# Kernel optimization log

Hardware: AMD Instinct MI355X
Metric: run time of the kernel (lower is better)

The kernel has to match this reference:

```python
import jax, jax.numpy as jnp
import numpy as np

EMB, NW, H, L, FF, VOCAB, BS = 512, 64, 8, 4, 2048, 50257, 16


def setup_inputs() -> dict:
    key = jax.random.key(0)
    ks = jax.random.split(key, 8)
    d = EMB
    def n(k, shape, s=0.02):
        return jax.random.normal(k, shape, jnp.float32) * s
    return {
        "w_emb": jax.random.normal(ks[0], (BS, NW, d), jnp.float32),
        "table": jax.random.normal(ks[1], (VOCAB, d), jnp.float32) * 0.02,
        "word_enc": n(ks[2], (NW + 1, d)),            # learned token encodings
        "Wqkv": n(ks[3], (L, 3 * d, d)),              # in_proj per layer
        "bqkv": jnp.zeros((L, 3 * d), jnp.float32),
        "Wo": n(ks[4], (L, d, d)),
        "bo": jnp.zeros((L, d), jnp.float32),
        "W1": n(ks[5], (L, FF, d)),
        "b1": jnp.zeros((L, FF), jnp.float32),
        "W2": n(ks[6], (L, d, FF)),
        "b2": jnp.zeros((L, d), jnp.float32),
        "g1": jnp.ones((L, d), jnp.float32),
        "be1": jnp.zeros((L, d), jnp.float32),
        "g2": jnp.ones((L, d), jnp.float32),
        "be2": jnp.zeros((L, d), jnp.float32),
    }


def _ln(x, g, b, eps=1e-5):
    m = x.mean(-1, keepdims=True)
    v = ((x - m) ** 2).mean(-1, keepdims=True)
    return (x - m) * jax.lax.rsqrt(v + eps) * g + b


def reference(w_emb, table, word_enc, Wqkv, bqkv, Wo, bo, W1, b1, W2, b2, g1, be1, g2, be2):
    bs, _, d = w_emb.shape
    dh = d // H
    scale = 1.0 / np.sqrt(dh).astype(np.float32)
    # prepend zero token, add learned encodings -> (bs, NW+1, d)
    x = jnp.concatenate([jnp.zeros((bs, 1, d), w_emb.dtype), w_emb], axis=1) + word_enc
    for l in range(L):
        # self-attention (post-LN TransformerEncoderLayer, ReLU FFN)
        qkv = x @ Wqkv[l].T + bqkv[l]
        q, k, v = jnp.split(qkv, 3, axis=-1)
        s = x.shape[1]
        q = q.reshape(bs, s, H, dh)
        k = k.reshape(bs, s, H, dh)
        v = v.reshape(bs, s, H, dh)
        att = jax.nn.softmax(jnp.einsum('bqhd,bkhd->bhqk', q, k) * scale, axis=-1)
        ctx = jnp.einsum('bhqk,bkhd->bqhd', att, v).reshape(bs, s, d)
        x = _ln(x + ctx @ Wo[l].T + bo[l], g1[l], be1[l])
        h = jax.nn.relu(x @ W1[l].T + b1[l])
        x = _ln(x + h @ W2[l].T + b2[l], g2[l], be2[l])
    out = x[:, :-1]                                   # drop last position -> (bs, NW, d)
    # linear lookup: (out * table).sum(-1) == out @ table.T
    return jnp.einsum('bnd,vd->bnv', out, table)
```

## Files before the change

### kernel.cpp

```cpp
#include <hip/hip_runtime.h>
#include <hip/hip_bf16.h>

#define EMB 512
#define NW  64
#define SEQ 65
#define NH  8
#define DH  64
#define NL  4
#define FF_ 2048
#define VOCAB 50257
#define BS  16
#define TOK (BS*SEQ)
#define TOUT (BS*NW)

typedef short short8  __attribute__((ext_vector_type(8)));
typedef unsigned short ushort8n __attribute__((ext_vector_type(8)));
typedef float f32x4   __attribute__((ext_vector_type(4)));

__device__ __forceinline__ unsigned short f2bf(float f) {
    unsigned u = __float_as_uint(f);
    return (unsigned short)((u + 0x7FFF + ((u >> 16) & 1)) >> 16);
}

template<int N> __device__ __forceinline__ void wait_vm() {
    asm volatile("s_waitcnt vmcnt(%0)" :: "n"(N) : "memory");
}

constexpr int ilog2c(int v) { return v == 32 ? 5 : v == 64 ? 6 : v == 128 ? 7 : 0; }

#define SZ_WQKV (NL*3*EMB*EMB)
#define SZ_WO   (NL*EMB*EMB)
#define SZ_W1   (NL*FF_*EMB)
#define SZ_W2   (NL*EMB*FF_)
#define SZ_TAB  (VOCAB*EMB)
#define CVT_TOTAL (SZ_WQKV+SZ_WO+SZ_W1+SZ_W2+SZ_TAB)
#define O_WO   (SZ_WQKV)
#define O_W1   (O_WO+SZ_WO)
#define O_W2   (O_W1+SZ_W1)
#define O_TAB  (O_W2+SZ_W2)

__global__ void cvt_kernel(const float* __restrict__ wqkv, const float* __restrict__ wo,
                           const float* __restrict__ w1, const float* __restrict__ w2,
                           const float* __restrict__ table, unsigned short* __restrict__ dst) {
    const int U = CVT_TOTAL / 8;
    for (int u = blockIdx.x * blockDim.x + threadIdx.x; u < U; u += gridDim.x * blockDim.x) {
        size_t elem = (size_t)u * 8;
        const float* src; size_t loc = elem;
        if      (elem < O_WO)  { src = wqkv; }
        else if (elem < O_W1)  { src = wo;    loc = elem - O_WO; }
        else if (elem < O_W2)  { src = w1;    loc = elem - O_W1; }
        else if (elem < O_TAB) { src = w2;    loc = elem - O_W2; }
        else                   { src = table; loc = elem - O_TAB; }
        float4 f0 = *(const float4*)(src + loc);
        float4 f1 = *(const float4*)(src + loc + 4);
        ushort8n o;
        o[0]=f2bf(f0.x); o[1]=f2bf(f0.y); o[2]=f2bf(f0.z); o[3]=f2bf(f0.w);
        o[4]=f2bf(f1.x); o[5]=f2bf(f1.y); o[6]=f2bf(f1.z); o[7]=f2bf(f1.w);
        *(ushort8n*)(dst + elem) = o;
    }
}

__global__ void embed_kernel(const float* __restrict__ w_emb,
                             const float* __restrict__ word_enc,
                             float* __restrict__ x32,
                             unsigned short* __restrict__ x16) {
    int idx = blockIdx.x * blockDim.x + threadIdx.x;
    const int total = BS * SEQ * EMB;
    if (idx >= total) return;
    int d = idx & (EMB - 1);
    int s = (idx >> 9) % SEQ;
    int b = idx / (SEQ * EMB);
    float we = word_enc[s * EMB + d];
    float e = (s == 0) ? 0.f : w_emb[((size_t)b * NW + (s - 1)) * EMB + d];
    float v = e + we;
    x32[idx] = v;
    x16[idx] = f2bf(v);
}

template<int TM, int TN, int BK, int OUT_BF16, int RELU, int COMPACT, int SPLITK>
__global__ __launch_bounds__(256) void gemm4(const unsigned short* __restrict__ A,
                                             const unsigned short* __restrict__ B,
                                             const float* __restrict__ bias,
                                             void* __restrict__ C0,
                                             void* __restrict__ C1,
                                             const float* __restrict__ res,
                                             int M, int N, int K, int lda, int ldb) {
    constexpr int LTM = ilog2c(TM);
    constexpr int LTN = ilog2c(TN);
    constexpr int FR  = TM / 32, FC = TN / 32;
    constexpr int WRH = TM / 2,  WCH = TN / 2;
    constexpr int KCH = BK / 32;
    constexpr int AI  = (TM * BK) / (8 * 256);
    constexpr int BI  = (TN * BK) / (8 * 256);
    constexpr int L   = AI + BI;
    constexpr int ASZ = TM * BK * 2;
    constexpr int STRIDE = (TM + TN) * BK * 2;
    __shared__ __align__(16) char smem[3 * STRIDE];

    int t = threadIdx.x;
    int w = t >> 6, l = t & 63;
    int wr = w >> 1, wc = w & 1;
    int lr = l & 15, lh = l >> 4;

    int mtiles = (M + TM - 1) / TM;
    int ntiles = (N + TN - 1) / TN;
    int bid = blockIdx.x;
    int nchunk = gridDim.x >> 3;
    int lin = (bid & 7) * nchunk + (bid >> 3);
    int part = 0;
    if (SPLITK) { int tpp = mtiles * ntiles; part = (lin >= tpp); lin -= part * tpp; }
    int m0 = (lin % mtiles) * TM;
    int n0 = (lin / mtiles) * TN;

    const unsigned short* Ap = A + (size_t)part * K;
    const unsigned short* Bp = B + (size_t)part * K;
    float* Cf = (float*)(part ? C1 : C0);
    const float* biasp = (SPLITK && part) ? nullptr : bias;
    const float* resp  = (SPLITK && part) ? nullptr : res;

    f32x4 acc[FR][FC] = {};
    const int nt = K / BK;

    auto stageA = [&](int kt, int p) {
        char* dst = smem + p * STRIDE;
        #pragma unroll
        for (int i = 0; i < AI; ++i) {
            int tt = i * 256 + t;
            int row = tt & (TM - 1);
            int slot = tt >> LTM;
            int gr = m0 + row;
            if (COMPACT) gr = ((gr >> 6) * SEQ) + (gr & 63);
            else if (gr >= M) gr = M - 1;
            const unsigned short* gp = Ap + (size_t)gr * lda + kt + slot * 8;
            __builtin_amdgcn_global_load_lds(
                (const __attribute__((address_space(1))) void*)gp,
                (__attribute__((address_space(3))) void*)(dst + (size_t)(i * 256 + w * 64) * 16),
                16, 0, 0);
        }
    };
    auto stageB = [&](int kt, int p) {
        char* dst = smem + p * STRIDE + ASZ;
        #pragma unroll
        for (int i = 0; i < BI; ++i) {
            int tt = i * 256 + t;
            int row = tt & (TN - 1);
            int slot = tt >> LTN;
            int gr = n0 + row;
            if (gr >= N) gr = N - 1;
            const unsigned short* gp = Bp + (size_t)gr * ldb + kt + slot * 8;
            __builtin_amdgcn_global_load_lds(
                (const __attribute__((address_space(1))) void*)gp,
                (__attribute__((address_space(3))) void*)(dst + (size_t)(i * 256 + w * 64) * 16),
                16, 0, 0);
        }
    };
    auto compute = [&](int p) {
        const unsigned short* as_ = (const unsigned short*)(smem + p * STRIDE);
        const unsigned short* bs_ = as_ + TM * BK;
        #pragma unroll
        for (int kk = 0; kk < KCH; ++kk) {
            short8 af[FR], bfv[FC];
            #pragma unroll
            for (int mi = 0; mi < FR; ++mi)
                af[mi] = *(const short8*)(as_ + ((size_t)(kk * 4 + lh) * TM + wr * WRH + mi * 16 + lr) * 8);
            #pragma unroll
            for (int ni = 0; ni < FC; ++ni)
                bfv[ni] = *(const short8*)(bs_ + ((size_t)(kk * 4 + lh) * TN + wc * WCH + ni * 16 + lr) * 8);
            #pragma unroll
            for (int mi = 0; mi < FR; ++mi)
                #pragma unroll
                for (int ni = 0; ni < FC; ++ni)
                    acc[mi][ni] = __builtin_amdgcn_mfma_f32_16x16x32_bf16(af[mi], bfv[ni], acc[mi][ni], 0, 0, 0);
        }
    };

    stageA(0, 0); stageB(0, 0);
    if (nt > 1) { stageA(BK, 1); stageB(BK, 1); }

    for (int it = 0; it < nt; ++it) {
        if (it + 1 < nt) wait_vm<L>(); else wait_vm<0>();
        __builtin_amdgcn_s_barrier();
        __builtin_amdgcn_sched_barrier(0);
        if (it + 2 < nt) {
            stageA((it + 2) * BK, (it + 2) % 3);
            stageB((it + 2) * BK, (it + 2) % 3);
        }
        __builtin_amdgcn_s_setprio(1);
        compute(it % 3);
        __builtin_amdgcn_s_setprio(0);
        __builtin_amdgcn_sched_barrier(0);
    }

    if (OUT_BF16) {
        #pragma unroll
        for (int ni = 0; ni < FC; ++ni) {
            int gcol = n0 + wc * WCH + ni * 16 + lr;
            if (gcol >= N) continue;
            float bv = biasp ? biasp[gcol] : 0.f;
            #pragma unroll
            for (int mi = 0; mi < FR; ++mi)
                #pragma unroll
                for (int r = 0; r < 4; ++r) {
                    int grow = m0 + wr * WRH + mi * 16 + lh * 4 + r;
                    if (grow >= M) continue;
                    float v = acc[mi][ni][r] + bv;
                    if (RELU) v = fmaxf(v, 0.f);
                    ((unsigned short*)C0)[(size_t)grow * N + gcol] = f2bf(v);
                }
        }
    } else {
        __syncthreads();
        constexpr int PAD = WCH + 4;
        constexpr int CPR = WCH / 4;
        constexpr int J   = (16 * CPR) / 64;
        float* ep = (float*)smem + (size_t)w * 16 * PAD;
        #pragma unroll
        for (int mi = 0; mi < FR; ++mi) {
            asm volatile("s_waitcnt lgkmcnt(0)" ::: "memory");
            __builtin_amdgcn_sched_barrier(0);
            #pragma unroll
            for (int ni = 0; ni < FC; ++ni)
                #pragma unroll
                for (int r = 0; r < 4; ++r)
                    ep[(lh * 4 + r) * PAD + ni * 16 + lr] = acc[mi][ni][r];
            asm volatile("s_waitcnt lgkmcnt(0)" ::: "memory");
            __builtin_amdgcn_sched_barrier(0);
            #pragma unroll
            for (int j = 0; j < J; ++j) {
                int f4  = j * 64 + l;
                int row = f4 / CPR;
                int c4  = f4 % CPR;
                int grow = m0 + wr * WRH + mi * 16 + row;
                int gc   = n0 + wc * WCH + c4 * 4;
                if (grow < M) {
                    float4 v = *(const float4*)(ep + row * PAD + c4 * 4);
                    if (gc + 3 < N) {
                        if (biasp) {
                            float4 b4 = *(const float4*)(biasp + gc);
                            v.x += b4.x; v.y += b4.y; v.z += b4.z; v.w += b4.w;
                        }
                        if (resp) {
                            const float* rp = resp + (size_t)grow * N + gc;
                            v.x += rp[0]; v.y += rp[1]; v.z += rp[2]; v.w += rp[3];
                        }
                        if (RELU) {
                            v.x = fmaxf(v.x, 0.f); v.y = fmaxf(v.y, 0.f);
                            v.z = fmaxf(v.z, 0.f); v.w = fmaxf(v.w, 0.f);
                        }
                        *(float4*)(Cf + (size_t)grow * N + gc) = v;
                    } else {
                        const float* pv = (const float*)&v;
                        #pragma unroll
                        for (int e = 0; e < 4; ++e)
                            if (gc + e < N) {
                                float vv = pv[e];
                                if (biasp) vv += biasp[gc + e];
                                if (resp)  vv += resp[(size_t)grow * N + gc + e];
                                if (RELU)  vv = fmaxf(vv, 0.f);
                                Cf[(size_t)grow * N + gc + e] = vv;
                            }
                    }
                }
            }
        }
    }
}

template<int TM, int TN, int OUT_BF16, int RELU, int COMPACT>
__global__ __launch_bounds__(256) void gemm2(const unsigned short* __restrict__ A,
                                             const float* __restrict__ B,
                                             const float* __restrict__ bias,
                                             void* __restrict__ C,
                                             int M, int N, int K) {
    constexpr int LTM = (TM == 128) ? 7 : 6;
    constexpr int FR  = TM / 32, FC = TN / 32;
    constexpr int WRH = TM / 2,  WCH = TN / 2;
    constexpr int AI  = TM / 64;
    constexpr int TPR = 256 / TN;
    constexpr int SPT = 4 / TPR;
    constexpr int STRIDE = (TM + TN) * 64;
    __shared__ __align__(16) char smem[2 * STRIDE];

    int t = threadIdx.x;
    int w = t >> 6, l = t & 63;
    int wr = w >> 1, wc = w & 1;
    int lr = l & 15, lh = l >> 4;
    int m0 = blockIdx.y * TM, n0 = blockIdx.x * TN;

    int br = t / TPR, bh = t % TPR;
    int gbr = n0 + br; if (gbr >= N) gbr = N - 1;
    const float* bbase = B + (size_t)gbr * K + bh * (SPT * 8);

    f32x4  acc[FR][FC] = {};
    float4 breg[TN / 32];
    const int nt = K >> 5;

    auto stageA = [&](int kt, int p) {
        char* dst = smem + p * STRIDE;
        #pragma unroll
        for (int i = 0; i < AI; ++i) {
            int tt   = i * 256 + t;
            int row  = tt & (TM - 1);
            int slot = tt >> LTM;
            int gr   = m0 + row;
            if (COMPACT) gr = ((gr >> 6) * SEQ) + (gr & 63);
            else if (gr >= M) gr = M - 1;
            const unsigned short* gp = A + (size_t)gr * K + kt + slot * 8;
            __builtin_amdgcn_global_load_lds(
                (const __attribute__((address_space(1))) void*)gp,
                (__attribute__((address_space(3))) void*)(dst + (size_t)(i * 256 + w * 64) * 16),
                16, 0, 0);
        }
    };
    auto loadB = [&](int kt) {
        const float* bp = bbase + kt;
        #pragma unroll
        for (int j = 0; j < TN / 32; ++j) breg[j] = *(const float4*)(bp + j * 4);
    };
    auto writeB = [&](int p) {
        unsigned short* bs = (unsigned short*)(smem + p * STRIDE + TM * 64);
        #pragma unroll
        for (int s = 0; s < SPT; ++s) {
            ushort8n u;
            #pragma unroll
            for (int e = 0; e < 8; ++e) {
                float f = ((const float*)&breg[s * 2 + (e >> 2)])[e & 3];
                u[e] = f2bf(f);
            }
            int slot = bh * SPT + s;
            *(ushort8n*)(bs + ((size_t)slot * TN + br) * 8) = u;
        }
    };
    auto compute = [&](int p) {
        const unsigned short* as_ = (const unsigned short*)(smem + p * STRIDE);
        const unsigned short* bs_ = as_ + TM * 32;
        short8 af[FR], bfv[FC];
        #pragma unroll
        for (int mi = 0; mi < FR; ++mi)
            af[mi] = *(const short8*)(as_ + ((size_t)lh * TM + wr * WRH + mi * 16 + lr) * 8);
        #pragma unroll
        for (int ni = 0; ni < FC; ++ni)
            bfv[ni] = *(const short8*)(bs_ + ((size_t)lh * TN + wc * WCH + ni * 16 + lr) * 8);
        #pragma unroll
        for (int mi = 0; mi < FR; ++mi)
            #pragma unroll
            for (int ni = 0; ni < FC; ++ni)
                acc[mi][ni] = __builtin_amdgcn_mfma_f32_16x16x32_bf16(af[mi], bfv[ni], acc[mi][ni], 0, 0, 0);
    };

    stageA(0, 0); loadB(0); writeB(0);
    __syncthreads();
    for (int it = 0; it < nt; ++it) {
        int p = it & 1;
        if (it + 1 < nt) { stageA((it + 1) << 5, 1 - p); loadB((it + 1) << 5); }
        compute(p);
        if (it + 1 < nt) writeB(1 - p);
        __syncthreads();
    }

    #pragma unroll
    for (int ni = 0; ni < FC; ++ni) {
        int gcol = n0 + wc * WCH + ni * 16 + lr;
        if (gcol >= N) continue;
        float bv = bias ? bias[gcol] : 0.f;
        #pragma unroll
        for (int mi = 0; mi < FR; ++mi)
            #pragma unroll
            for (int r = 0; r < 4; ++r) {
                int grow = m0 + wr * WRH + mi * 16 + lh * 4 + r;
                if (grow >= M) continue;
                float v = acc[mi][ni][r] + bv;
                if (RELU) v = fmaxf(v, 0.f);
                if (OUT_BF16) ((unsigned short*)C)[(size_t)grow * N + gcol] = f2bf(v);
                else          ((float*)C)[(size_t)grow * N + gcol] = v;
            }
    }
}

#define APAD 65
__global__ __launch_bounds__(256) void attn_fused(const float* __restrict__ qkv,
                                                  unsigned short* __restrict__ ctx16) {
    int qpart = blockIdx.x;
    int h = blockIdx.y, b = blockIdx.z;
    __shared__ float Ks[SEQ * APAD];
    __shared__ float Vs[SEQ * APAD];
    __shared__ float qsh[4][64];
    __shared__ float pws[4][SEQ + 3];

    const float* base = qkv + (size_t)b * SEQ * (3 * EMB) + h * DH;
    int t = threadIdx.x;
    for (int idx = t; idx < SEQ * 16; idx += 256) {
        int r = idx >> 4, c4 = (idx & 15) << 2;
        const float* rp = base + (size_t)r * (3 * EMB);
        float4 kv = *(const float4*)(rp + EMB + c4);
        float4 vv = *(const float4*)(rp + 2 * EMB + c4);
        float* kd = Ks + r * APAD + c4;
        kd[0] = kv.x; kd[1] = kv.y; kd[2] = kv.z; kd[3] = kv.w;
        float* vd = Vs + r * APAD + c4;
        vd[0] = vv.x; vd[1] = vv.y; vd[2] = vv.z; vd[3] = vv.w;
    }
    __syncthreads();

    int w = t >> 6, l = t & 63;
    int qstart = qpart ? 33 : 0;
    int qend   = qpart ? SEQ : 33;
    for (int qi = qstart + w; qi < qend; qi += 4) {
        qsh[w][l] = base[(size_t)qi * (3 * EMB) + l];
        float s = 0.f;
        #pragma unroll 16
        for (int d = 0; d < DH; ++d) s += qsh[w][d] * Ks[l * APAD + d];
        s *= 0.125f;
        float s64 = -1e30f;
        if (l == 0) {
            float acc64 = 0.f;
            #pragma unroll 16
            for (int d = 0; d < DH; ++d) acc64 += qsh[w][d] * Ks[64 * APAD + d];
            s64 = acc64 * 0.125f;
        }
        float m = (l == 0) ? fmaxf(s, s64) : s;
        #pragma unroll
        for (int off = 32; off >= 1; off >>= 1) m = fmaxf(m, __shfl_xor(m, off));
        float e = __expf(s - m);
        pws[w][l] = e;
        float esum = e;
        if (l == 0) { float e64 = __expf(s64 - m); pws[w][64] = e64; esum += e64; }
        #pragma unroll
        for (int off = 32; off >= 1; off >>= 1) esum += __shfl_xor(esum, off);
        float inv = 1.f / esum;
        float acc = 0.f;
        #pragma unroll 13
        for (int j = 0; j < SEQ; ++j) acc += pws[w][j] * Vs[j * APAD + l];
        ctx16[((size_t)b * SEQ + qi) * EMB + h * DH + l] = f2bf(acc * inv);
    }
}

__global__ __launch_bounds__(128) void ln_kernel(const float* __restrict__ x,
                                                 const float* __restrict__ p,
                                                 const float* __restrict__ g,
                                                 const float* __restrict__ be,
                                                 float* __restrict__ y32,
                                                 unsigned short* __restrict__ y16) {
    int row = blockIdx.x;
    int t = threadIdx.x;
    const float4 xv = ((const float4*)(x + (size_t)row * EMB))[t];
    const float4 pv = ((const float4*)(p + (size_t)row * EMB))[t];
    float v0 = xv.x + pv.x, v1 = xv.y + pv.y, v2 = xv.z + pv.z, v3 = xv.w + pv.w;
    float sum = v0 + v1 + v2 + v3;
    float sq  = v0 * v0 + v1 * v1 + v2 * v2 + v3 * v3;
    #pragma unroll
    for (int off = 32; off >= 1; off >>= 1) {
        sum += __shfl_down(sum, off);
        sq  += __shfl_down(sq,  off);
    }
    __shared__ float s0[2], s1[2];
    if ((t & 63) == 0) { s0[t >> 6] = sum; s1[t >> 6] = sq; }
    __syncthreads();
    float S = s0[0] + s0[1], Q = s1[0] + s1[1];
    float mean = S * (1.f / EMB);
    float var  = Q * (1.f / EMB) - mean * mean;
    float rstd = rsqrtf(var + 1e-5f);
    const float4 gv = ((const float4*)g)[t];
    const float4 bv = ((const float4*)be)[t];
    float4 o;
    o.x = (v0 - mean) * rstd * gv.x + bv.x;
    o.y = (v1 - mean) * rstd * gv.y + bv.y;
    o.z = (v2 - mean) * rstd * gv.z + bv.z;
    o.w = (v3 - mean) * rstd * gv.w + bv.w;
    ((float4*)(y32 + (size_t)row * EMB))[t] = o;
    ushort4 h;
    h.x = f2bf(o.x); h.y = f2bf(o.y); h.z = f2bf(o.z); h.w = f2bf(o.w);
    ((ushort4*)(y16 + (size_t)row * EMB))[t] = h;
}

extern "C" void kernel_launch(void* const* d_in, const int* in_sizes, int n_in,
                              void* d_out, int out_size, void* d_ws, size_t ws_size,
                              hipStream_t stream) {
    const float* w_emb    = (const float*)d_in[0];
    const float* table    = (const float*)d_in[1];
    const float* word_enc = (const float*)d_in[2];
    const float* Wqkv     = (const float*)d_in[3];
    const float* bqkv     = (const float*)d_in[4];
    const float* Wo       = (const float*)d_in[5];
    const float* bo       = (const float*)d_in[6];
    const float* W1       = (const float*)d_in[7];
    const float* b1       = (const float*)d_in[8];
    const float* W2       = (const float*)d_in[9];
    const float* b2       = (const float*)d_in[10];
    const float* g1       = (const float*)d_in[11];
    const float* be1      = (const float*)d_in[12];
    const float* g2       = (const float*)d_in[13];
    const float* be2      = (const float*)d_in[14];
    float* out = (float*)d_out;

    const size_t act_bytes = (size_t)TOK * EMB * 4 * 3
                           + (size_t)TOK * 3 * EMB * 4
                           + (size_t)TOK * EMB * 2 * 3
                           + (size_t)TOK * FF_ * 2;
    const size_t wgt_bytes = (size_t)CVT_TOTAL * 2;
    const bool fast = ws_size >= act_bytes + wgt_bytes;

    char* ws = (char*)d_ws;
    unsigned short* wgt16 = nullptr;
    if (fast) { wgt16 = (unsigned short*)ws; ws += wgt_bytes; }
    float* xa32  = (float*)ws;                    ws += (size_t)TOK * EMB * 4;
    float* xb32  = (float*)ws;                    ws += (size_t)TOK * EMB * 4;
    float* qkv32 = (float*)ws;                    ws += (size_t)TOK * 3 * EMB * 4;
    float* proj32= (float*)ws;                    ws += (size_t)TOK * EMB * 4;
    unsigned short* hbuf16= (unsigned short*)ws;  ws += (size_t)TOK * FF_ * 2;
    unsigned short* xa16  = (unsigned short*)ws;  ws += (size_t)TOK * EMB * 2;
    unsigned short* xb16  = (unsigned short*)ws;  ws += (size_t)TOK * EMB * 2;
    unsigned short* ctx16 = (unsigned short*)ws;  ws += (size_t)TOK * EMB * 2;
    float* projb  = qkv32;

    if (fast) cvt_kernel<<<2048, 256, 0, stream>>>(Wqkv, Wo, W1, W2, table, wgt16);

    {
        int total = BS * SEQ * EMB;
        embed_kernel<<<(total + 255) / 256, 256, 0, stream>>>(w_emb, word_enc, xa32, xa16);
    }

    if (fast) {
        const unsigned short* wq16 = wgt16;
        const unsigned short* wo16 = wgt16 + O_WO;
        const unsigned short* w116 = wgt16 + O_W1;
        const unsigned short* w216 = wgt16 + O_W2;
        const unsigned short* tab16= wgt16 + O_TAB;

        for (int l = 0; l < NL; ++l) {
            gemm4<64,64,64,0,0,0,0><<<dim3(408), 256, 0, stream>>>(
                xa16, wq16 + (size_t)l * 3 * EMB * EMB, bqkv + (size_t)l * 3 * EMB,
                qkv32, nullptr, nullptr, TOK, 3 * EMB, EMB, EMB, EMB);
            attn_fused<<<dim3(2, NH, BS), 256, 0, stream>>>(qkv32, ctx16);
            gemm4<64,32,64,0,0,0,1><<<dim3(544), 256, 0, stream>>>(
                ctx16, wo16 + (size_t)l * EMB * EMB, bo + (size_t)l * EMB,
                proj32, projb, xa32, TOK, EMB, 256, EMB, EMB);
            ln_kernel<<<TOK, 128, 0, stream>>>(proj32, projb,
                g1 + (size_t)l * EMB, be1 + (size_t)l * EMB, xb32, xb16);
            gemm4<64,64,64,1,1,0,0><<<dim3(544), 256, 0, stream>>>(
                xb16, w116 + (size_t)l * FF_ * EMB, b1 + (size_t)l * FF_,
                hbuf16, nullptr, nullptr, TOK, FF_, EMB, EMB, EMB);
            gemm4<64,32,64,0,0,0,1><<<dim3(544), 256, 0, stream>>>(
                hbuf16, w216 + (size_t)l * EMB * FF_, b2 + (size_t)l * EMB,
                proj32, projb, xb32, TOK, EMB, 1024, FF_, FF_);
            ln_kernel<<<TOK, 128, 0, stream>>>(proj32, projb,
                g2 + (size_t)l * EMB, be2 + (size_t)l * EMB, xa32, xa16);
        }
        gemm4<128,128,32,0,0,1,0><<<dim3(3144), 256, 0, stream>>>(
            xa16, tab16, nullptr, out, nullptr, nullptr, TOUT, VOCAB, EMB, EMB, EMB);
    } else {
        for (int l = 0; l < NL; ++l) {
            const float* Wqkv_l = Wqkv + (size_t)l * 3 * EMB * EMB;
            const float* Wo_l   = Wo   + (size_t)l * EMB * EMB;
            const float* W1_l   = W1   + (size_t)l * FF_ * EMB;
            const float* W2_l   = W2   + (size_t)l * EMB * FF_;
            gemm2<64,64,0,0,0><<<dim3((3 * EMB) / 64, (TOK + 63) / 64), 256, 0, stream>>>(
                xa16, Wqkv_l, bqkv + (size_t)l * 3 * EMB, qkv32, TOK, 3 * EMB, EMB);
            attn_fused<<<dim3(2, NH, BS), 256, 0, stream>>>(qkv32, ctx16);
            gemm2<64,64,0,0,0><<<dim3(EMB / 64, (TOK + 63) / 64), 256, 0, stream>>>(
                ctx16, Wo_l, bo + (size_t)l * EMB, proj32, TOK, EMB, EMB);
            ln_kernel<<<TOK, 128, 0, stream>>>(xa32, proj32, g1 + (size_t)l * EMB, be1 + (size_t)l * EMB, xb32, xb16);
            gemm2<64,64,1,1,0><<<dim3(FF_ / 64, (TOK + 63) / 64), 256, 0, stream>>>(
                xb16, W1_l, b1 + (size_t)l * FF_, hbuf16, TOK, FF_, EMB);
            gemm2<64,64,0,0,0><<<dim3(EMB / 64, (TOK + 63) / 64), 256, 0, stream>>>(
                hbuf16, W2_l, b2 + (size_t)l * EMB, proj32, TOK, EMB, FF_);
            ln_kernel<<<TOK, 128, 0, stream>>>(xb32, proj32, g2 + (size_t)l * EMB, be2 + (size_t)l * EMB, xa32, xa16);
        }
        gemm2<128,128,0,0,1><<<dim3((VOCAB + 127) / 128, TOUT / 128), 256, 0, stream>>>(
            xa16, table, nullptr, out, TOUT, VOCAB, EMB);
    }
}
```

Baseline: 515.3 us.

## Add 256x256 tile triple-buffered GEMM kernel for vocab projection

New measurement: 511.2 us (median of 2 runs). No clear change (-0.8%).

```diff
diff --git a/kernel.cpp b/kernel.cpp
--- a/kernel.cpp
+++ b/kernel.cpp
@@ -266,6 +266,135 @@
     }
 }
 
+__global__ __launch_bounds__(512) void gemm5(const unsigned short* __restrict__ A,
+                                             const unsigned short* __restrict__ B,
+                                             float* __restrict__ C,
+                                             int M, int N, int K) {
+    constexpr int TM = 256, TN = 256, BK = 32;
+    constexpr int AI = 2, BI = 2, L = 4;
+    constexpr int ASZ = TM * BK * 2;
+    constexpr int STRIDE = (TM + TN) * BK * 2;
+    __shared__ __align__(16) char smem[3 * STRIDE];
+
+    int t = threadIdx.x;
+    int w = t >> 6, l = t & 63;
+    int wr = w >> 2, wc = w & 3;
+    int lr = l & 15, lh = l >> 4;
+
+    int nwg = gridDim.x;
+    int q = nwg >> 3, r = nwg & 7;
+    int bid = blockIdx.x;
+    int xcd = bid & 7, i0 = bid >> 3;
+    int lin = (xcd < r ? xcd * (q + 1) : r * (q + 1) + (xcd - r) * q) + i0;
+    int mtiles = (M + TM - 1) / TM;
+    int m0 = (lin % mtiles) * TM;
+    int n0 = (lin / mtiles) * TN;
+
+    f32x4 acc[8][4] = {};
+    const int nt = K / BK;
+
+    auto stageA = [&](int kt, int p) {
+        char* dst = smem + p * STRIDE;
+        #pragma unroll
+        for (int i = 0; i < AI; ++i) {
+            int tt = i * 512 + t;
+            int row = tt & (TM - 1);
+            int slot = tt >> 8;
+            int gr = m0 + row;
+            gr = ((gr >> 6) * SEQ) + (gr & 63);
+            const unsigned short* gp = A + (size_t)gr * K + kt + slot * 8;
+            __builtin_amdgcn_global_load_lds(
+                (const __attribute__((address_space(1))) void*)gp,
+                (__attribute__((address_space(3))) void*)(dst + (size_t)(i * 512 + w * 64) * 16),
+                16, 0, 0);
+        }
+    };
+    auto stageB = [&](int kt, int p) {
+        char* dst = smem + p * STRIDE + ASZ;
+        #pragma unroll
+        for (int i = 0; i < BI; ++i) {
+            int tt = i * 512 + t;
+            int row = tt & (TN - 1);
+            int slot = tt >> 8;
+            int gr = n0 + row;
+            if (gr >= N) gr = N - 1;
+            const unsigned short* gp = B + (size_t)gr * K + kt + slot * 8;
+            __builtin_amdgcn_global_load_lds(
+                (const __attribute__((address_space(1))) void*)gp,
+                (__attribute__((address_space(3))) void*)(dst + (size_t)(i * 512 + w * 64) * 16),
+                16, 0, 0);
+        }
+    };
+    auto compute = [&](int p) {
+        const unsigned short* as_ = (const unsigned short*)(smem + p * STRIDE);
+        const unsigned short* bs_ = as_ + TM * BK;
+        short8 af[8], bf[4];
+        #pragma unroll
+        for (int mi = 0; mi < 8; ++mi)
+            af[mi] = *(const short8*)(as_ + ((size_t)lh * TM + wr * 128 + mi * 16 + lr) * 8);
+        #pragma unroll
+        for (int ni = 0; ni < 4; ++ni)
+            bf[ni] = *(const short8*)(bs_ + ((size_t)lh * TN + wc * 64 + ni * 16 + lr) * 8);
+        #pragma unroll
+        for (int mi = 0; mi < 8; ++mi)
+            #pragma unroll
+            for (int ni = 0; ni < 4; ++ni)
+                acc[mi][ni] = __builtin_amdgcn_mfma_f32_16x16x32_bf16(af[mi], bf[ni], acc[mi][ni], 0, 0, 0);
+    };
+
+    stageA(0, 0); stageB(0, 0);
+    if (nt > 1) { stageA(BK, 1); stageB(BK, 1); }
+
+    for (int it = 0; it < nt; ++it) {
+        if (it + 1 < nt) wait_vm<L>(); else wait_vm<0>();
+        __builtin_amdgcn_s_barrier();
+        __builtin_amdgcn_sched_barrier(0);
+        if (it + 2 < nt) {
+            stageA((it + 2) * BK, (it + 2) % 3);
+            stageB((it + 2) * BK, (it + 2) % 3);
+        }
+        __builtin_amdgcn_s_setprio(1);
+        compute(it % 3);
+        __builtin_amdgcn_s_setprio(0);
+        __builtin_amdgcn_sched_barrier(0);
+    }
+
+    __syncthreads();
+    constexpr int PAD = 68;
+    float* ep = (float*)smem + (size_t)w * 16 * PAD;
+    #pragma unroll
+    for (int mi = 0; mi < 8; ++mi) {
+        asm volatile("s_waitcnt lgkmcnt(0)" ::: "memory");
+        __builtin_amdgcn_sched_barrier(0);
+        #pragma unroll
+        for (int ni = 0; ni < 4; ++ni)
+            #pragma unroll
+            for (int rr = 0; rr < 4; ++rr)
+                ep[(lh * 4 + rr) * PAD + ni * 16 + lr] = acc[mi][ni][rr];
+        asm volatile("s_waitcnt lgkmcnt(0)" ::: "memory");
+        __builtin_amdgcn_sched_barrier(0);
+        #pragma unroll
+        for (int j = 0; j < 4; ++j) {
+            int f4  = j * 64 + l;
+            int row = f4 >> 4;
+            int c4  = f4 & 15;
+            int grow = m0 + wr * 128 + mi * 16 + row;
+            int gc   = n0 + wc * 64 + c4 * 4;
+            if (grow < M) {
+                float4 v = *(const float4*)(ep + row * PAD + c4 * 4);
+                if (gc + 3 < N) {
+                    *(float4*)(C + (size_t)grow * N + gc) = v;
+                } else {
+                    const float* pv = (const float*)&v;
+                    #pragma unroll
+                    for (int e = 0; e < 4; ++e)
+                        if (gc + e < N) C[(size_t)grow * N + gc + e] = pv[e];
+                }
+            }
+        }
+    }
+}
+
 template<int TM, int TN, int OUT_BF16, int RELU, int COMPACT>
 __global__ __launch_bounds__(256) void gemm2(const unsigned short* __restrict__ A,
                                              const float* __restrict__ B,
@@ -545,8 +674,8 @@
             ln_kernel<<<TOK, 128, 0, stream>>>(proj32, projb,
                 g2 + (size_t)l * EMB, be2 + (size_t)l * EMB, xa32, xa16);
         }
-        gemm4<128,128,32,0,0,1,0><<<dim3(3144), 256, 0, stream>>>(
-            xa16, tab16, nullptr, out, nullptr, nullptr, TOUT, VOCAB, EMB, EMB, EMB);
+        gemm5<<<dim3(4 * ((VOCAB + 255) / 256)), 512, 0, stream>>>(
+            xa16, tab16, out, TOUT, VOCAB, EMB);
     } else {
         for (int l = 0; l < NL; ++l) {
             const float* Wqkv_l = Wqkv + (size_t)l * 3 * EMB * EMB;
```
